# Kernel optimization log

Measured on AMD Instinct MI355X. Metric: run time of the kernel, lower is better.

The kernel has to match this reference:

```python
import jax, jax.numpy as jnp
import numpy as np

B, T, C = 2, 2048, 2048
N_HEAD = 16
N_KV_HEAD = 16
HEAD_DIM = C // N_HEAD  # 128
KV_LORA = C // 2        # 1024
KV_PE = KV_LORA // 4    # 256
KV_CONTENT = KV_LORA - KV_PE  # 768
EPS = 1.1920929e-07  # torch.finfo(float32).eps, F.rms_norm default


def _rms_norm(x):
    # unlearned RMSNorm over last dim
    return x * jax.lax.rsqrt(jnp.mean(x * x, axis=-1, keepdims=True) + EPS)


def _apply_rotary(x, cos, sin):
    # x: (B,T,H,D); cos,sin: (1,T,1,D/2)
    d = x.shape[-1] // 2
    x1, x2 = x[..., :d], x[..., d:]
    return jnp.concatenate([x1 * cos + x2 * sin, -x1 * sin + x2 * cos], axis=-1)


def setup_inputs() -> dict:
    key = jax.random.key(0)
    ks = jax.random.split(key, 9)
    x = jax.random.normal(ks[0], (B, T, C), dtype=jnp.float32)
    # realistic RoPE tables (values bounded like real cos/sin)
    half = HEAD_DIM // 2
    inv_freq = 1.0 / (10000.0 ** (np.arange(0, half, dtype=np.float32) / half))
    tpos = np.arange(T, dtype=np.float32)
    ang = np.einsum('t,d->td', tpos, inv_freq)
    cos = jnp.asarray(np.cos(ang))[None, :, None, :]
    sin = jnp.asarray(np.sin(ang))[None, :, None, :]
    s = 0.02
    wq_a = jax.random.normal(ks[1], (C, KV_LORA), dtype=jnp.float32) * s
    wq_b = jax.random.normal(ks[2], (KV_LORA, N_HEAD * HEAD_DIM), dtype=jnp.float32) * s
    wkv_a = jax.random.normal(ks[3], (C, KV_LORA), dtype=jnp.float32) * s
    wk_b = jax.random.normal(ks[4], (KV_CONTENT, N_KV_HEAD * HEAD_DIM), dtype=jnp.float32) * s
    wkpe_b = jax.random.normal(ks[5], (KV_PE, N_KV_HEAD * HEAD_DIM), dtype=jnp.float32) * s
    wv_b = jax.random.normal(ks[6], (KV_CONTENT, N_KV_HEAD * HEAD_DIM), dtype=jnp.float32) * s
    wo = jax.random.normal(ks[7], (C, C), dtype=jnp.float32) * s
    return dict(x=x, cos=cos, sin=sin, wq_a=wq_a, wq_b=wq_b, wkv_a=wkv_a,
                wk_b=wk_b, wkpe_b=wkpe_b, wv_b=wv_b, wo=wo)


def reference(x, cos, sin, wq_a, wq_b, wkv_a, wk_b, wkpe_b, wv_b, wo):
    Bx, Tx, Cx = x.shape
    # low-rank Q path
    q = (x @ wq_a) @ wq_b                      # (B,T,H*D)
    q = q.reshape(Bx, Tx, N_HEAD, HEAD_DIM)
    # low-rank KV path with pe/content split
    kv_latent = x @ wkv_a                       # (B,T,KV_LORA)
    kv_pe = kv_latent[..., :KV_PE]
    kv_content = kv_latent[..., KV_PE:]
    k_content = (kv_content @ wk_b).reshape(Bx, Tx, N_KV_HEAD, HEAD_DIM)
    k_pe = (kv_pe @ wkpe_b).reshape(Bx, Tx, N_KV_HEAD, HEAD_DIM)
    k = k_content + _apply_rotary(k_pe, cos, sin)
    v = (kv_content @ wv_b).reshape(Bx, Tx, N_KV_HEAD, HEAD_DIM)
    # QK RMSNorm (unlearned)
    q = _rms_norm(q)
    k = _rms_norm(k)
    # SDPA, causal (kv_cache=None path); n_head == n_kv_head
    qh = q.transpose(0, 2, 1, 3)  # (B,H,T,D)
    kh = k.transpose(0, 2, 1, 3)
    vh = v.transpose(0, 2, 1, 3)
    scale = 1.0 / jnp.sqrt(jnp.asarray(HEAD_DIM, dtype=x.dtype))
    scores = jnp.einsum('bhqd,bhkd->bhqk', qh, kh) * scale
    causal = jnp.tril(jnp.ones((Tx, Tx), dtype=bool))
    scores = jnp.where(causal[None, None], scores, jnp.asarray(-jnp.inf, dtype=scores.dtype))
    probs = jax.nn.softmax(scores, axis=-1)
    y = jnp.einsum('bhqk,bhkd->bhqd', probs, vh)
    y = y.transpose(0, 2, 1, 3).reshape(Bx, Tx, Cx)
    return y @ wo
```

## Files before the change

### kernel.cpp

```cpp
#include <hip/hip_runtime.h>
#include <cstddef>
#include <cstdint>

#define TT 2048
#define HH 16
#define EPSV 1.1920929e-07f
#define QSCALE 0.08838834764831845f
#define LOG2E 1.4426950408889634f
#define THRL 11.0f

typedef short bfv8 __attribute__((ext_vector_type(8)));
typedef float f32x4 __attribute__((ext_vector_type(4)));

__device__ __forceinline__ short f2bf(float f) {
    unsigned u = __builtin_bit_cast(unsigned, f);
    u += 0x7FFFu + ((u >> 16) & 1u);
    return (short)(u >> 16);
}
__device__ __forceinline__ float bf2f(short s) {
    unsigned u = ((unsigned)(unsigned short)s) << 16;
    return __builtin_bit_cast(float, u);
}
__device__ __forceinline__ bfv8 pack8(const float4 a, const float4 b) {
    bfv8 r;
    r[0]=f2bf(a.x); r[1]=f2bf(a.y); r[2]=f2bf(a.z); r[3]=f2bf(a.w);
    r[4]=f2bf(b.x); r[5]=f2bf(b.y); r[6]=f2bf(b.z); r[7]=f2bf(b.w);
    return r;
}
__device__ __forceinline__ void gload16(const void* g, void* l) {
    __builtin_amdgcn_global_load_lds(
        (const __attribute__((address_space(1))) unsigned int*)g,
        (__attribute__((address_space(3))) unsigned int*)l, 16, 0, 0);
}

__global__ __launch_bounds__(256) void convx(const float* __restrict__ src,
                                             short* __restrict__ dst, int n8)
{
    int i = blockIdx.x * blockDim.x + threadIdx.x;
    int stride = gridDim.x * blockDim.x;
    for (; i < n8; i += stride) {
        float4 a = ((const float4*)src)[2*i], b = ((const float4*)src)[2*i+1];
        ((bfv8*)dst)[i] = pack8(a, b);
    }
}

__global__ __launch_bounds__(256) void wtrans(const float* __restrict__ src,
                                              short* __restrict__ dst, int R, int C)
{
    __shared__ short tile[64][72];
    const int tid = threadIdx.x;
    const int r0 = blockIdx.y * 64, c0 = blockIdx.x * 64;
    {
        const int i = tid >> 2, c = (tid & 3) * 16;
        const float* sp = src + ((size_t)(r0 + i)) * C + c0 + c;
        float4 v0 = ((const float4*)sp)[0], v1 = ((const float4*)sp)[1];
        float4 v2 = ((const float4*)sp)[2], v3 = ((const float4*)sp)[3];
        *(bfv8*)&tile[i][c]     = pack8(v0, v1);
        *(bfv8*)&tile[i][c + 8] = pack8(v2, v3);
    }
    __syncthreads();
    {
        const int j = tid >> 2, rc = (tid & 3) * 16;
        bfv8 g0, g1;
#pragma unroll
        for (int jj = 0; jj < 8; ++jj) { g0[jj] = tile[rc + jj][j]; g1[jj] = tile[rc + 8 + jj][j]; }
        short* dp = dst + ((size_t)(c0 + j)) * R + r0 + rc;
        *(bfv8*)dp       = g0;
        *(bfv8*)(dp + 8) = g1;
    }
}

template<int OUT_MODE>
__global__ __launch_bounds__(256) void gemm_bf16(
    const short* __restrict__ A, int lda,
    const short* __restrict__ B, int ldb,
    void* __restrict__ Cptr, int ldc, int K)
{
    __shared__ short As[2][128 * 32];
    __shared__ short Bs[2][128 * 32];
    const int tid = threadIdx.x;
    const int w = tid >> 6, lane = tid & 63;
    const int lr = lane & 15, lg = lane >> 4;
    const int wr = w >> 1, wc = w & 1;
    const size_t bm = (size_t)blockIdx.y * 128, bn = (size_t)blockIdx.x * 128;

    f32x4 acc[4][4] = {};

    const int r0 = tid >> 2, ch = (tid & 3) * 8;
    const short* aB0 = A + (bm + r0) * (size_t)lda + ch;
    const short* aB1 = aB0 + 64 * (size_t)lda;
    const short* bB0 = B + (bn + r0) * (size_t)ldb + ch;
    const short* bB1 = bB0 + 64 * (size_t)ldb;
    const int wof = w * 512;

    gload16(aB0, As[0] + wof);
    gload16(aB1, As[0] + wof + 2048);
    gload16(bB0, Bs[0] + wof);
    gload16(bB1, Bs[0] + wof + 2048);
    __syncthreads();

    int cur = 0;
    for (int k0 = 0; k0 < K; k0 += 32) {
        if (k0 + 32 < K) {
            gload16(aB0 + k0 + 32, As[cur ^ 1] + wof);
            gload16(aB1 + k0 + 32, As[cur ^ 1] + wof + 2048);
            gload16(bB0 + k0 + 32, Bs[cur ^ 1] + wof);
            gload16(bB1 + k0 + 32, Bs[cur ^ 1] + wof + 2048);
        }
        bfv8 af[4], bfr[4];
#pragma unroll
        for (int i = 0; i < 4; ++i) {
            af[i]  = *(const bfv8*)&As[cur][(wr * 64 + i * 16 + lr) * 32 + lg * 8];
            bfr[i] = *(const bfv8*)&Bs[cur][(wc * 64 + i * 16 + lr) * 32 + lg * 8];
        }
#pragma unroll
        for (int i = 0; i < 4; ++i)
#pragma unroll
            for (int j = 0; j < 4; ++j)
                acc[i][j] = __builtin_amdgcn_mfma_f32_16x16x32_bf16(af[i], bfr[j], acc[i][j], 0, 0, 0);
        __syncthreads();
        cur ^= 1;
    }

    const size_t crow = bm + wr * 64 + 4 * lg;
    const size_t ccol = bn + wc * 64 + lr;
#pragma unroll
    for (int i = 0; i < 4; ++i)
#pragma unroll
        for (int j = 0; j < 4; ++j)
#pragma unroll
            for (int r = 0; r < 4; ++r) {
                size_t off = (crow + i * 16 + r) * (size_t)ldc + ccol + j * 16;
                if (OUT_MODE == 0) ((float*)Cptr)[off] = acc[i][j][r];
                else               ((short*)Cptr)[off] = f2bf(acc[i][j][r]);
            }
}

__global__ __launch_bounds__(256) void finalize_k(
    const short* __restrict__ kc, const short* __restrict__ pe,
    const float* __restrict__ cosb, const float* __restrict__ sinb,
    short* __restrict__ kb)
{
    const int gw = blockIdx.x * 4 + (threadIdx.x >> 6);
    const int l = threadIdx.x & 63;
    const int r = gw >> 4, h = gw & 15;
    const int t = r & (TT - 1), b = r >> 11;
    const size_t kcb = (size_t)r * 4096 + h * 128;
    const size_t peb = (size_t)r * 2048 + h * 128;

    float x1 = bf2f(pe[peb + l]), x2 = bf2f(pe[peb + 64 + l]);
    float c = cosb[t * 64 + l], s = sinb[t * 64 + l];
    float lo = bf2f(kc[kcb + l])      + x1 * c + x2 * s;
    float hi = bf2f(kc[kcb + 64 + l]) - x1 * s + x2 * c;

    float ss = lo * lo + hi * hi;
#pragma unroll
    for (int o = 32; o; o >>= 1) ss += __shfl_xor(ss, o);
    float rr = rsqrtf(ss * (1.0f / 128.0f) + EPSV);
    const size_t ob = (((size_t)b * HH + h) * TT + t) * 128;
    kb[ob + l]      = f2bf(lo * rr);
    kb[ob + 64 + l] = f2bf(hi * rr);
}

__global__ __launch_bounds__(256) void finalize_q(
    const short* __restrict__ qi, short* __restrict__ qo)
{
    const int gw = blockIdx.x * 4 + (threadIdx.x >> 6);
    const int l = threadIdx.x & 63;
    const int r = gw >> 4, h = gw & 15;
    const int t = r & (TT - 1), b = r >> 11;
    const short* qp = qi + (size_t)r * 2048 + h * 128 + 2 * l;
    float a = bf2f(qp[0]), bq = bf2f(qp[1]);
    float ss = a * a + bq * bq;
#pragma unroll
    for (int o = 32; o; o >>= 1) ss += __shfl_xor(ss, o);
    float rr = rsqrtf(ss * (1.0f / 128.0f) + EPSV) * (QSCALE * LOG2E);
    short* op = qo + (((size_t)b * HH + h) * TT + t) * 128 + 2 * l;
    op[0] = f2bf(a * rr);
    op[1] = f2bf(bq * rr);
}

__global__ __launch_bounds__(256) void vtrans(
    const short* __restrict__ src, short* __restrict__ dst)
{
    __shared__ short tile[64][72];
    const int tt = blockIdx.x, dt = blockIdx.y, bh = blockIdx.z;
    const int tid = threadIdx.x;
    {
        const int i = tid >> 2, c = (tid & 3) * 16;
        const size_t sb = ((size_t)((bh >> 4) * TT + tt * 64 + i)) * 4096 + 2048 + (bh & 15) * 128 + dt * 64 + c;
        *(bfv8*)&tile[i][c]     = *(const bfv8*)&src[sb];
        *(bfv8*)&tile[i][c + 8] = *(const bfv8*)&src[sb + 8];
    }
    __syncthreads();
    {
        const int j = tid >> 2, rc = (tid & 3) * 16;
        bfv8 g0, g1;
#pragma unroll
        for (int jj = 0; jj < 8; ++jj) { g0[jj] = tile[rc + jj][j]; g1[jj] = tile[rc + 8 + jj][j]; }
        const size_t db = (((size_t)bh) * 128 + dt * 64 + j) * TT + tt * 64 + rc;
        *(bfv8*)&dst[db]     = g0;
        *(bfv8*)&dst[db + 8] = g1;
    }
}

__device__ __forceinline__ void qk_tile(const short* __restrict__ Ks,
    const bfv8 aq[4], f32x4 s[4], int lr, int lg)
{
#pragma unroll
    for (int ct = 0; ct < 4; ++ct) {
        f32x4 a = {0.f, 0.f, 0.f, 0.f};
        const int row = ct * 16 + lr;
#pragma unroll
        for (int ks = 0; ks < 4; ++ks) {
            const bfv8 bk = *(const bfv8*)&Ks[row * 128 + (((ks * 4 + lg) ^ (row & 7)) * 8)];
            a = __builtin_amdgcn_mfma_f32_16x16x32_bf16(aq[ks], bk, a, 0, 0, 0);
        }
        s[ct] = a;
    }
}

__device__ __forceinline__ void mask_diag(f32x4 s[4], int lr, int lg, int w)
{
    const int rq = w * 16 + 4 * lg;
#pragma unroll
    for (int ct = 0; ct < 4; ++ct)
#pragma unroll
        for (int r = 0; r < 4; ++r)
            if (ct * 16 + lr > rq + r) s[ct][r] = -__builtin_inff();
}

__device__ __forceinline__ void softmax1(f32x4 s[4], float m[4], float l[4], f32x4 o[8])
{
    float mt[4];
#pragma unroll
    for (int r = 0; r < 4; ++r) mt[r] = fmaxf(fmaxf(s[0][r], s[1][r]), fmaxf(s[2][r], s[3][r]));
#pragma unroll
    for (int off = 1; off < 16; off <<= 1)
#pragma unroll
        for (int r = 0; r < 4; ++r) mt[r] = fmaxf(mt[r], __shfl_xor(mt[r], off));
    float g = fmaxf(fmaxf(mt[0] - m[0], mt[1] - m[1]), fmaxf(mt[2] - m[2], mt[3] - m[3]));
    if (!__all(g <= THRL)) {
        float alpha[4];
#pragma unroll
        for (int r = 0; r < 4; ++r) {
            float mn = fmaxf(m[r], mt[r]);
            alpha[r] = exp2f(m[r] - mn);
            m[r] = mn; l[r] *= alpha[r];
        }
#pragma unroll
        for (int dt = 0; dt < 8; ++dt) {
            o[dt][0] *= alpha[0]; o[dt][1] *= alpha[1];
            o[dt][2] *= alpha[2]; o[dt][3] *= alpha[3];
        }
    }
#pragma unroll
    for (int ct = 0; ct < 4; ++ct)
#pragma unroll
        for (int r = 0; r < 4; ++r) s[ct][r] = exp2f(s[ct][r] - m[r]);
    float rs[4];
#pragma unroll
    for (int r = 0; r < 4; ++r) rs[r] = (s[0][r] + s[1][r]) + (s[2][r] + s[3][r]);
#pragma unroll
    for (int off = 1; off < 16; off <<= 1)
#pragma unroll
        for (int r = 0; r < 4; ++r) rs[r] += __shfl_xor(rs[r], off);
#pragma unroll
    for (int r = 0; r < 4; ++r) l[r] += rs[r];
}

__device__ __forceinline__ void softmax2(
    f32x4 s1[4], f32x4 s2[4],
    float m1[4], float l1[4], float m2[4], float l2[4],
    f32x4 o1[8], f32x4 o2[8])
{
    float mt1[4], mt2[4];
#pragma unroll
    for (int r = 0; r < 4; ++r) {
        mt1[r] = fmaxf(fmaxf(s1[0][r], s1[1][r]), fmaxf(s1[2][r], s1[3][r]));
        mt2[r] = fmaxf(fmaxf(s2[0][r], s2[1][r]), fmaxf(s2[2][r], s2[3][r]));
    }
#pragma unroll
    for (int off = 1; off < 16; off <<= 1)
#pragma unroll
        for (int r = 0; r < 4; ++r) {
            mt1[r] = fmaxf(mt1[r], __shfl_xor(mt1[r], off));
            mt2[r] = fmaxf(mt2[r], __shfl_xor(mt2[r], off));
        }
    float g1 = fmaxf(fmaxf(mt1[0] - m1[0], mt1[1] - m1[1]), fmaxf(mt1[2] - m1[2], mt1[3] - m1[3]));
    float g2 = fmaxf(fmaxf(mt2[0] - m2[0], mt2[1] - m2[1]), fmaxf(mt2[2] - m2[2], mt2[3] - m2[3]));
    if (!__all(g1 <= THRL)) {
        float alpha[4];
#pragma unroll
        for (int r = 0; r < 4; ++r) {
            float mn = fmaxf(m1[r], mt1[r]);
            alpha[r] = exp2f(m1[r] - mn);
            m1[r] = mn; l1[r] *= alpha[r];
        }
#pragma unroll
        for (int dt = 0; dt < 8; ++dt) {
            o1[dt][0] *= alpha[0]; o1[dt][1] *= alpha[1];
            o1[dt][2] *= alpha[2]; o1[dt][3] *= alpha[3];
        }
    }
    if (!__all(g2 <= THRL)) {
        float alpha[4];
#pragma unroll
        for (int r = 0; r < 4; ++r) {
            float mn = fmaxf(m2[r], mt2[r]);
            alpha[r] = exp2f(m2[r] - mn);
            m2[r] = mn; l2[r] *= alpha[r];
        }
#pragma unroll
        for (int dt = 0; dt < 8; ++dt) {
            o2[dt][0] *= alpha[0]; o2[dt][1] *= alpha[1];
            o2[dt][2] *= alpha[2]; o2[dt][3] *= alpha[3];
        }
    }
#pragma unroll
    for (int ct = 0; ct < 4; ++ct)
#pragma unroll
        for (int r = 0; r < 4; ++r) {
            s1[ct][r] = exp2f(s1[ct][r] - m1[r]);
            s2[ct][r] = exp2f(s2[ct][r] - m2[r]);
        }
    float rs1[4], rs2[4];
#pragma unroll
    for (int r = 0; r < 4; ++r) {
        rs1[r] = (s1[0][r] + s1[1][r]) + (s1[2][r] + s1[3][r]);
        rs2[r] = (s2[0][r] + s2[1][r]) + (s2[2][r] + s2[3][r]);
    }
#pragma unroll
    for (int off = 1; off < 16; off <<= 1)
#pragma unroll
        for (int r = 0; r < 4; ++r) {
            rs1[r] += __shfl_xor(rs1[r], off);
            rs2[r] += __shfl_xor(rs2[r], off);
        }
#pragma unroll
    for (int r = 0; r < 4; ++r) { l1[r] += rs1[r]; l2[r] += rs2[r]; }
}

__device__ __forceinline__ void pv_tile(const short* __restrict__ Vs,
    short (&Psw)[16][72], const f32x4 s[4], f32x4 o[8], int lr, int lg)
{
#pragma unroll
    for (int ct = 0; ct < 4; ++ct)
#pragma unroll
        for (int r = 0; r < 4; ++r)
            Psw[4 * lg + r][ct * 16 + lr] = f2bf(s[ct][r]);
    const bfv8 pa0 = *(const bfv8*)&Psw[lr][lg * 8];
    const bfv8 pa1 = *(const bfv8*)&Psw[lr][32 + lg * 8];
#pragma unroll
    for (int dt = 0; dt < 8; ++dt) {
        const int row = dt * 16 + lr;
        const bfv8 bv0 = *(const bfv8*)&Vs[row * 64 + ((lg ^ (row & 7)) * 8)];
        const bfv8 bv1 = *(const bfv8*)&Vs[row * 64 + (((4 + lg) ^ (row & 7)) * 8)];
        o[dt] = __builtin_amdgcn_mfma_f32_16x16x32_bf16(pa0, bv0, o[dt], 0, 0, 0);
        o[dt] = __builtin_amdgcn_mfma_f32_16x16x32_bf16(pa1, bv1, o[dt], 0, 0, 0);
    }
}

__global__ __launch_bounds__(256) void attn_kernel(
    const short* __restrict__ qg, const short* __restrict__ kg,
    const short* __restrict__ vg, short* __restrict__ y)
{
    __shared__ short Ks[2][64 * 128];
    __shared__ short Vs[2][128 * 64];
    __shared__ short Ps[4][16][72];

    const int lin = blockIdx.x + 16 * blockIdx.y + 256 * blockIdx.z;
    const int work = (lin & 7) * 64 + (lin >> 3);
    const int pi = work & 15, h = (work >> 4) & 15, b = work >> 8;
    const int qt1 = pi, qt2 = 31 - pi;
    const int tid = threadIdx.x, w = tid >> 6, lane = tid & 63;
    const int lr = lane & 15, lg = lane >> 4;

    const size_t tok0 = ((size_t)b * HH + h) * TT;
    bfv8 aq1[4], aq2[4];
    {
        const size_t q1 = (tok0 + qt1 * 64 + w * 16 + lr) * 128;
        const size_t q2 = (tok0 + qt2 * 64 + w * 16 + lr) * 128;
#pragma unroll
        for (int ks = 0; ks < 4; ++ks) {
            aq1[ks] = *(const bfv8*)&qg[q1 + ks * 32 + lg * 8];
            aq2[ks] = *(const bfv8*)&qg[q2 + ks * 32 + lg * 8];
        }
    }
    f32x4 o1[8] = {}; f32x4 o2[8] = {};
    float m1[4], l1[4], m2[4], l2[4];
#pragma unroll
    for (int r = 0; r < 4; ++r) { m1[r] = m2[r] = -__builtin_inff(); l1[r] = l2[r] = 0.f; }

    const size_t vhead = ((size_t)b * HH + h) * (size_t)128 * TT;
    const int krow = tid >> 4, kub = tid & 15;
    const int vrow = tid >> 3, vub = tid & 7;
    const int wof = w * 512;

#define STAGE_KV(KT, BUF)                                                          \
    {                                                                              \
        const size_t kbase = (tok0 + (KT) * 64) * 128;                             \
        _Pragma("unroll")                                                          \
        for (int p = 0; p < 4; ++p) {                                              \
            int row = p * 16 + krow;                                               \
            int u = kub ^ (row & 7);                                               \
            gload16(kg + kbase + row * 128 + u * 8, Ks[BUF] + wof + p * 2048);     \
            int rv = p * 32 + vrow;                                                \
            int uv = vub ^ (rv & 7);                                               \
            gload16(vg + vhead + (size_t)rv * TT + (KT) * 64 + uv * 8,             \
                    Vs[BUF] + wof + p * 2048);                                     \
        }                                                                          \
    }

    STAGE_KV(0, 0);
    __syncthreads();

    int cur = 0;
    for (int kt = 0; kt <= qt1; ++kt) {
        if (kt < qt2) STAGE_KV(kt + 1, cur ^ 1);
        f32x4 s1[4], s2[4];
        qk_tile(Ks[cur], aq2, s2, lr, lg);
        qk_tile(Ks[cur], aq1, s1, lr, lg);
        if (kt == qt1) mask_diag(s1, lr, lg, w);
        softmax2(s1, s2, m1, l1, m2, l2, o1, o2);
        pv_tile(Vs[cur], Ps[w], s2, o2, lr, lg);
        pv_tile(Vs[cur], Ps[w], s1, o1, lr, lg);
        __syncthreads();
        cur ^= 1;
    }
    for (int kt = qt1 + 1; kt <= qt2; ++kt) {
        if (kt < qt2) STAGE_KV(kt + 1, cur ^ 1);
        f32x4 s2[4];
        qk_tile(Ks[cur], aq2, s2, lr, lg);
        if (kt == qt2) mask_diag(s2, lr, lg, w);
        softmax1(s2, m2, l2, o2);
        pv_tile(Vs[cur], Ps[w], s2, o2, lr, lg);
        __syncthreads();
        cur ^= 1;
    }

#pragma unroll
    for (int r = 0; r < 4; ++r) {
        float inv1 = 1.0f / l1[r], inv2 = 1.0f / l2[r];
        const size_t y1 = ((size_t)b * TT + qt1 * 64 + w * 16 + 4 * lg + r) * 2048 + h * 128 + lr;
        const size_t y2 = ((size_t)b * TT + qt2 * 64 + w * 16 + 4 * lg + r) * 2048 + h * 128 + lr;
#pragma unroll
        for (int dt = 0; dt < 8; ++dt) {
            y[y1 + dt * 16] = f2bf(o1[dt][r] * inv1);
            y[y2 + dt * 16] = f2bf(o2[dt][r] * inv2);
        }
    }
}

extern "C" void kernel_launch(void* const* d_in, const int* in_sizes, int n_in,
                              void* d_out, int out_size, void* d_ws, size_t ws_size,
                              hipStream_t stream)
{
    const float* x      = (const float*)d_in[0];
    const float* cosb   = (const float*)d_in[1];
    const float* sinb   = (const float*)d_in[2];
    const float* wq_a   = (const float*)d_in[3];
    const float* wq_b   = (const float*)d_in[4];
    const float* wkv_a  = (const float*)d_in[5];
    const float* wk_b   = (const float*)d_in[6];
    const float* wkpe_b = (const float*)d_in[7];
    const float* wv_b   = (const float*)d_in[8];
    const float* wo     = (const float*)d_in[9];

    short* wsp = (short*)d_ws;
    short* W1  = wsp;
    short* W2  = wsp + 4194304;
    short* W3  = wsp + 7340032;
    short* W4  = wsp + 7864320;
    short* W5  = wsp + 9961472;
    short* C1  = wsp + 14155776;
    short* KV2 = wsp + 22544384;
    short* KPE = wsp + 39321600;
    short* KB  = wsp + 47710208;
    short* VB  = wsp + 56098816;
    short* XB  = (short*)d_out;

    dim3 blk(256);

    convx<<<2048, blk, 0, stream>>>(x, XB, 1048576);
    wtrans<<<dim3(16, 32), blk, 0, stream>>>(wq_a,   W1,                2048, 1024);
    wtrans<<<dim3(16, 32), blk, 0, stream>>>(wkv_a,  W1 + 1024 * 2048,  2048, 1024);
    wtrans<<<dim3(32, 12), blk, 0, stream>>>(wk_b,   W2,                 768, 2048);
    wtrans<<<dim3(32, 12), blk, 0, stream>>>(wv_b,   W2 + 2048 * 768,    768, 2048);
    wtrans<<<dim3(32,  4), blk, 0, stream>>>(wkpe_b, W3,                 256, 2048);
    wtrans<<<dim3(32, 16), blk, 0, stream>>>(wq_b,   W4,                1024, 2048);
    wtrans<<<dim3(32, 32), blk, 0, stream>>>(wo,     W5,                2048, 2048);

    gemm_bf16<1><<<dim3(16, 32), blk, 0, stream>>>(XB, 2048, W1, 2048, C1, 2048, 2048);
    gemm_bf16<1><<<dim3(32, 32), blk, 0, stream>>>(C1 + 1280, 2048, W2, 768, KV2, 4096, 768);
    gemm_bf16<1><<<dim3(16, 32), blk, 0, stream>>>(C1 + 1024, 2048, W3, 256, KPE, 2048, 256);

    finalize_k<<<16384, blk, 0, stream>>>(KV2, KPE, cosb, sinb, KB);
    vtrans<<<dim3(32, 2, 32), blk, 0, stream>>>(KV2, VB);

    gemm_bf16<1><<<dim3(16, 32), blk, 0, stream>>>(C1, 2048, W4, 1024, KPE, 2048, 1024);
    finalize_q<<<16384, blk, 0, stream>>>(KPE, KV2);

    attn_kernel<<<dim3(16, 16, 2), blk, 0, stream>>>(KV2, KB, VB, C1);

    gemm_bf16<0><<<dim3(16, 32), blk, 0, stream>>>(C1, 2048, W5, 2048, d_out, 2048, 2048);
}
```

Baseline: 357.1 us.

## Replace GEMM with 256x128-tile 8-wave kernel using swizzled LDS and split prefetch

Replaces the 128x128, 4-wave bf16 GEMM with a 512-thread kernel that computes 256x128 output tiles over K-chunks of 64. The LDS layout gets an XOR swizzle, and the next chunk's loads are issued in two halves interleaved with the MFMA phases using explicit vmcnt waits and raw barriers. It also remaps workgroup IDs for cache locality and raises wave priority around the MFMA blocks. The aim is better data reuse per block, fewer LDS bank conflicts and better latency hiding, at the cost of more LDS per block and fewer blocks in each GEMM grid.

```diff
diff --git a/kernel.cpp b/kernel.cpp
--- a/kernel.cpp
+++ b/kernel.cpp
@@ -71,69 +71,114 @@
 }
 
 template<int OUT_MODE>
-__global__ __launch_bounds__(256) void gemm_bf16(
+__global__ __launch_bounds__(512) void gemm8(
     const short* __restrict__ A, int lda,
     const short* __restrict__ B, int ldb,
     void* __restrict__ Cptr, int ldc, int K)
 {
-    __shared__ short As[2][128 * 32];
-    __shared__ short Bs[2][128 * 32];
+    constexpr int CH_B = 2;
+    constexpr int NCH  = 6;
+
+    __shared__ short Asm[2][256 * 64];
+    __shared__ short Bsm[2][128 * 64];
+
+    const int nwg = gridDim.x * gridDim.y;
+    int lin = blockIdx.y * gridDim.x + blockIdx.x;
+    lin = (lin & 7) * (nwg >> 3) + (lin >> 3);
+    const int bx = lin % gridDim.x, by = lin / gridDim.x;
+
     const int tid = threadIdx.x;
     const int w = tid >> 6, lane = tid & 63;
     const int lr = lane & 15, lg = lane >> 4;
     const int wr = w >> 1, wc = w & 1;
-    const size_t bm = (size_t)blockIdx.y * 128, bn = (size_t)blockIdx.x * 128;
+    const size_t bm = (size_t)by * 256, bn = (size_t)bx * 128;
+
+    const int crow = tid >> 3, cunit = tid & 7;
+    const short* Ag = A + (bm + crow) * (size_t)lda + (cunit ^ (crow & 7)) * 8;
+    const short* Bg = B + (bn + crow) * (size_t)ldb + (cunit ^ (crow & 7)) * 8;
+    const int ldsOff = crow * 64 + cunit * 8;
+
+    auto issue = [&](int ic, int kk, int bb) {
+        if (ic < CH_B)
+            gload16(Bg + (size_t)(ic * 64) * ldb + kk, &Bsm[bb][ic * 4096 + ldsOff]);
+        else
+            gload16(Ag + (size_t)((ic - CH_B) * 64) * lda + kk,
+                    &Asm[bb][(ic - CH_B) * 4096 + ldsOff]);
+    };
 
     f32x4 acc[4][4] = {};
 
-    const int r0 = tid >> 2, ch = (tid & 3) * 8;
-    const short* aB0 = A + (bm + r0) * (size_t)lda + ch;
-    const short* aB1 = aB0 + 64 * (size_t)lda;
-    const short* bB0 = B + (bn + r0) * (size_t)ldb + ch;
-    const short* bB1 = bB0 + 64 * (size_t)ldb;
-    const int wof = w * 512;
-
-    gload16(aB0, As[0] + wof);
-    gload16(aB1, As[0] + wof + 2048);
-    gload16(bB0, Bs[0] + wof);
-    gload16(bB1, Bs[0] + wof + 2048);
-    __syncthreads();
-
-    int cur = 0;
-    for (int k0 = 0; k0 < K; k0 += 32) {
-        if (k0 + 32 < K) {
-            gload16(aB0 + k0 + 32, As[cur ^ 1] + wof);
-            gload16(aB1 + k0 + 32, As[cur ^ 1] + wof + 2048);
-            gload16(bB0 + k0 + 32, Bs[cur ^ 1] + wof);
-            gload16(bB1 + k0 + 32, Bs[cur ^ 1] + wof + 2048);
-        }
-        bfv8 af[4], bfr[4];
+#pragma unroll
+    for (int ic = 0; ic < NCH; ++ic) issue(ic, 0, 0);
+
+    const int NT = K >> 6;
+    for (int t = 0; t < NT; ++t) {
+        const int c = t & 1, cn = c ^ 1;
+        const int kn = (t + 1) << 6;
+        const bool more = (t + 1 < NT);
+        bfv8 ah[4], bk[4];
+
+        if (more) {
+            issue(0, kn, cn); issue(1, kn, cn); issue(2, kn, cn);
+            asm volatile("s_waitcnt vmcnt(3)" ::: "memory");
+        } else {
+            asm volatile("s_waitcnt vmcnt(0)" ::: "memory");
+        }
+        __builtin_amdgcn_s_barrier();
+#pragma unroll
+        for (int j = 0; j < 4; ++j) {
+            const int row = wc * 64 + j * 16 + lr;
+            bk[j] = *(const bfv8*)&Bsm[c][row * 64 + ((lg ^ (row & 7)) * 8)];
+        }
 #pragma unroll
         for (int i = 0; i < 4; ++i) {
-            af[i]  = *(const bfv8*)&As[cur][(wr * 64 + i * 16 + lr) * 32 + lg * 8];
-            bfr[i] = *(const bfv8*)&Bs[cur][(wc * 64 + i * 16 + lr) * 32 + lg * 8];
-        }
+            const int row = wr * 64 + i * 16 + lr;
+            ah[i] = *(const bfv8*)&Asm[c][row * 64 + ((lg ^ (row & 7)) * 8)];
+        }
+        __builtin_amdgcn_s_setprio(1);
 #pragma unroll
         for (int i = 0; i < 4; ++i)
 #pragma unroll
             for (int j = 0; j < 4; ++j)
-                acc[i][j] = __builtin_amdgcn_mfma_f32_16x16x32_bf16(af[i], bfr[j], acc[i][j], 0, 0, 0);
-        __syncthreads();
-        cur ^= 1;
-    }
-
-    const size_t crow = bm + wr * 64 + 4 * lg;
-    const size_t ccol = bn + wc * 64 + lr;
-#pragma unroll
-    for (int i = 0; i < 4; ++i)
+                acc[i][j] = __builtin_amdgcn_mfma_f32_16x16x32_bf16(ah[i], bk[j], acc[i][j], 0, 0, 0);
+        __builtin_amdgcn_s_setprio(0);
+        __builtin_amdgcn_s_barrier();
+
+        if (more) { issue(3, kn, cn); issue(4, kn, cn); issue(5, kn, cn); }
+#pragma unroll
+        for (int j = 0; j < 4; ++j) {
+            const int row = wc * 64 + j * 16 + lr;
+            bk[j] = *(const bfv8*)&Bsm[c][row * 64 + (((4 + lg) ^ (row & 7)) * 8)];
+        }
+#pragma unroll
+        for (int i = 0; i < 4; ++i) {
+            const int row = wr * 64 + i * 16 + lr;
+            ah[i] = *(const bfv8*)&Asm[c][row * 64 + (((4 + lg) ^ (row & 7)) * 8)];
+        }
+        __builtin_amdgcn_s_barrier();
+        __builtin_amdgcn_s_setprio(1);
+#pragma unroll
+        for (int i = 0; i < 4; ++i)
+#pragma unroll
+            for (int j = 0; j < 4; ++j)
+                acc[i][j] = __builtin_amdgcn_mfma_f32_16x16x32_bf16(ah[i], bk[j], acc[i][j], 0, 0, 0);
+        __builtin_amdgcn_s_setprio(0);
+        __builtin_amdgcn_s_barrier();
+    }
+
+#pragma unroll
+    for (int i = 0; i < 4; ++i) {
+        const size_t r0 = bm + wr * 64 + i * 16 + 4 * lg;
+        const size_t c0 = bn + wc * 64 + lr;
 #pragma unroll
         for (int j = 0; j < 4; ++j)
 #pragma unroll
             for (int r = 0; r < 4; ++r) {
-                size_t off = (crow + i * 16 + r) * (size_t)ldc + ccol + j * 16;
+                const size_t off = (r0 + r) * (size_t)ldc + c0 + j * 16;
                 if (OUT_MODE == 0) ((float*)Cptr)[off] = acc[i][j][r];
                 else               ((short*)Cptr)[off] = f2bf(acc[i][j][r]);
             }
+    }
 }
 
 __global__ __launch_bounds__(256) void finalize_k(
@@ -481,6 +526,7 @@
     short* XB  = (short*)d_out;
 
     dim3 blk(256);
+    dim3 blk8(512);
 
     convx<<<2048, blk, 0, stream>>>(x, XB, 1048576);
     wtrans<<<dim3(16, 32), blk, 0, stream>>>(wq_a,   W1,                2048, 1024);
@@ -491,17 +537,17 @@
     wtrans<<<dim3(32, 16), blk, 0, stream>>>(wq_b,   W4,                1024, 2048);
     wtrans<<<dim3(32, 32), blk, 0, stream>>>(wo,     W5,                2048, 2048);
 
-    gemm_bf16<1><<<dim3(16, 32), blk, 0, stream>>>(XB, 2048, W1, 2048, C1, 2048, 2048);
-    gemm_bf16<1><<<dim3(32, 32), blk, 0, stream>>>(C1 + 1280, 2048, W2, 768, KV2, 4096, 768);
-    gemm_bf16<1><<<dim3(16, 32), blk, 0, stream>>>(C1 + 1024, 2048, W3, 256, KPE, 2048, 256);
+    gemm8<1><<<dim3(16, 16), blk8, 0, stream>>>(XB, 2048, W1, 2048, C1, 2048, 2048);
+    gemm8<1><<<dim3(32, 16), blk8, 0, stream>>>(C1 + 1280, 2048, W2, 768, KV2, 4096, 768);
+    gemm8<1><<<dim3(16, 16), blk8, 0, stream>>>(C1 + 1024, 2048, W3, 256, KPE, 2048, 256);
 
     finalize_k<<<16384, blk, 0, stream>>>(KV2, KPE, cosb, sinb, KB);
     vtrans<<<dim3(32, 2, 32), blk, 0, stream>>>(KV2, VB);
 
-    gemm_bf16<1><<<dim3(16, 32), blk, 0, stream>>>(C1, 2048, W4, 1024, KPE, 2048, 1024);
+    gemm8<1><<<dim3(16, 16), blk8, 0, stream>>>(C1, 2048, W4, 1024, KPE, 2048, 1024);
     finalize_q<<<16384, blk, 0, stream>>>(KPE, KV2);
 
     attn_kernel<<<dim3(16, 16, 2), blk, 0, stream>>>(KV2, KB, VB, C1);
 
-    gemm_bf16<0><<<dim3(16, 32), blk, 0, stream>>>(C1, 2048, W5, 2048, d_out, 2048, 2048);
-}
+    gemm8<0><<<dim3(16, 16), blk8, 0, stream>>>(C1, 2048, W5, 2048, d_out, 2048, 2048);
+}
```

Measured after the change: 407.8 us. +14.2%, slower.
